# Performance work log

Measured on AMD Instinct MI355X. Metric: run time of the kernel, lower is better.

Reference implementation:

```python
import jax, jax.numpy as jnp
import numpy as np

N_QUBITS = 4 + 4  # 8
N_LAYERS = 4
DIM = 2 ** N_QUBITS


def _apply_1q(state, U, wire):
    # state: (B, 2,...,2) complex; U: (2,2) complex; contract qubit `wire`
    s = jnp.moveaxis(state, wire + 1, -1)
    s = s @ U.T  # out[..., i] = sum_j U[i, j] * s[..., j]
    return jnp.moveaxis(s, -1, wire + 1)


def _apply_cnot(state, c, t):
    s = jnp.moveaxis(state, (c + 1, t + 1), (-2, -1))  # (..., 2c, 2t)
    s = jnp.concatenate([s[..., 0:1, :], s[..., 1:2, ::-1]], axis=-2)
    return jnp.moveaxis(s, (-2, -1), (c + 1, t + 1))


def _quantum_layer(q_in, qw):
    """Batched statevector sim: RY(pi*x) encoding + StronglyEntanglingLayers + <Z_i>."""
    B = q_in.shape[0]
    # RY(a)|0> = cos(a/2)|0> + sin(a/2)|1>, a = pi * x  -> product state
    half = q_in * (jnp.pi / 2)
    qvecs = jnp.stack([jnp.cos(half), jnp.sin(half)], axis=-1).astype(jnp.complex64)  # (B, n, 2)
    state = qvecs[:, 0]
    for i in range(1, N_QUBITS):
        state = (state[:, :, None] * qvecs[:, i][:, None, :]).reshape(B, -1)
    state = state.reshape((B,) + (2,) * N_QUBITS)
    # Rot(phi, theta, omega) = RZ(omega) RY(theta) RZ(phi)
    phi, theta, omega = qw[..., 0], qw[..., 1], qw[..., 2]
    c, s = jnp.cos(theta / 2), jnp.sin(theta / 2)
    m00 = jnp.exp(-0.5j * (phi + omega)) * c
    m01 = -jnp.exp(0.5j * (phi - omega)) * s
    m10 = jnp.exp(-0.5j * (phi - omega)) * s
    m11 = jnp.exp(0.5j * (phi + omega)) * c
    rot = jnp.stack([jnp.stack([m00, m01], -1), jnp.stack([m10, m11], -1)], -2)  # (L, n, 2, 2)
    rot = rot.astype(jnp.complex64)
    for l in range(N_LAYERS):
        for w in range(N_QUBITS):
            state = _apply_1q(state, rot[l, w], w)
        r = (l % (N_QUBITS - 1)) + 1  # PennyLane default ranges
        for w in range(N_QUBITS):
            state = _apply_cnot(state, w, (w + r) % N_QUBITS)
    amps = state.reshape(B, DIM)
    probs = jnp.real(amps * jnp.conj(amps))  # (B, 2^n) float32
    # <Z_i> = sum_b probs_b * (+1 if bit_i(b)==0 else -1); wire 0 = most significant axis
    idx = np.arange(DIM)
    bits = (idx[None, :] >> (N_QUBITS - 1 - np.arange(N_QUBITS))[:, None]) & 1  # (n, 2^n)
    zvals = jnp.asarray(1.0 - 2.0 * bits, dtype=jnp.float32)
    return probs @ zvals.T  # (B, n)


def _forward(x, w_pre1, b_pre1, w_pre2, b_pre2, w_pre3, b_pre3, qw,
             w_post1, b_post1, w_post2, b_post2, w_post3, b_post3):
    # eval mode: dropout is identity
    h = jax.nn.relu(x @ w_pre1 + b_pre1)
    h = jax.nn.relu(h @ w_pre2 + b_pre2)
    q_in = jnp.tanh(h @ w_pre3 + b_pre3)          # (B, n_qubits)
    z = _quantum_layer(q_in, qw)                   # (B, n_qubits)
    h = jax.nn.relu(z @ w_post1 + b_post1)
    h = jax.nn.relu(h @ w_post2 + b_post2)
    return h @ w_post3 + b_post3                   # (B, num_classes)


def setup_inputs() -> dict:
    key = jax.random.key(0)
    ks = jax.random.split(key, 16)
    B, D_IN, C = 16384, 41, 5
    def lin(k, fan_in, fan_out):
        lim = 1.0 / np.sqrt(fan_in)
        k1, k2 = jax.random.split(k)
        return (jax.random.uniform(k1, (fan_in, fan_out), jnp.float32, -lim, lim),
                jax.random.uniform(k2, (fan_out,), jnp.float32, -lim, lim))
    x = jax.random.normal(ks[0], (B, D_IN), jnp.float32)
    w_pre1, b_pre1 = lin(ks[1], D_IN, 64)
    w_pre2, b_pre2 = lin(ks[2], 64, 32)
    w_pre3, b_pre3 = lin(ks[3], 32, N_QUBITS)
    qw = jax.random.normal(ks[4], (N_LAYERS, N_QUBITS, 3), jnp.float32) * 0.1
    w_post1, b_post1 = lin(ks[5], N_QUBITS, 32)
    w_post2, b_post2 = lin(ks[6], 32, 16)
    w_post3, b_post3 = lin(ks[7], 16, C)
    return dict(x=x, w_pre1=w_pre1, b_pre1=b_pre1, w_pre2=w_pre2, b_pre2=b_pre2,
                w_pre3=w_pre3, b_pre3=b_pre3, qw=qw,
                w_post1=w_post1, b_post1=b_post1, w_post2=w_post2, b_post2=b_post2,
                w_post3=w_post3, b_post3=b_post3)


def reference(x, w_pre1, b_pre1, w_pre2, b_pre2, w_pre3, b_pre3, qw,
              w_post1, b_post1, w_post2, b_post2, w_post3, b_post3):
    return _forward(x, w_pre1, b_pre1, w_pre2, b_pre2, w_pre3, b_pre3, qw,
                    w_post1, b_post1, w_post2, b_post2, w_post3, b_post3)
```

## Files before the change

### kernel.cpp

```cpp
#include <hip/hip_runtime.h>
#include <math.h>

#define PI_HALF 1.57079632679489662f

typedef float v2f __attribute__((ext_vector_type(2)));


__device__ __forceinline__ v2f sp(float x) { v2f r; r.x = x; r.y = x; return r; }
__device__ __forceinline__ v2f pkfma(v2f a, v2f b, v2f c) {
  return __builtin_elementwise_fma(a, b, c);
}

template <int CTRL>
__device__ __forceinline__ float dpp_mov(float v) {
  int r = __builtin_amdgcn_update_dpp(0, __float_as_int(v), CTRL, 0xf, 0xf, true);
  return __int_as_float(r);
}
template <int MASK>
__device__ __forceinline__ float lane_xor(float v) {
  if constexpr (MASK == 1) return dpp_mov<0xB1>(v);
  else if constexpr (MASK == 2) return dpp_mov<0x4E>(v);
  else if constexpr (MASK == 8) return dpp_mov<0x128>(v);
  else return dpp_mov<0x1B>(dpp_mov<0x141>(v));
}
template <int MASK>
__device__ __forceinline__ v2f dpp2(v2f v) {
  v2f r; r.x = lane_xor<MASK>(v.x); r.y = lane_xor<MASK>(v.y); return r;
}

template <int W>
__device__ __forceinline__ void rot_lane(v2f (&RE)[8], v2f (&IM)[8],
                                         const float4 mA, int g) {
  constexpr int LM = 1 << (3 - W);
  const unsigned bit = (g >> (3 - W)) & 1u;
  const int sgn = (int)(bit << 31);
  v2f Av = sp(mA.x);
  v2f Bv = sp(__int_as_float(__float_as_int(mA.y) ^ sgn));
  v2f Cv = sp(__int_as_float(__float_as_int(mA.z) ^ sgn));
  v2f Dv = sp(mA.w);
#pragma unroll
  for (int j = 0; j < 8; ++j) {
    v2f pr = dpp2<LM>(RE[j]);
    v2f pi = dpp2<LM>(IM[j]);
    v2f nr = pkfma(-Dv, pi, pkfma(Cv, pr, pkfma(-Bv, IM[j], Av * RE[j])));
    v2f ni = pkfma( Dv, pr, pkfma(Cv, pi, pkfma( Bv, RE[j], Av * IM[j])));
    RE[j] = nr; IM[j] = ni;
  }
}

template <int JM>
__device__ __forceinline__ void rot_regj(v2f (&RE)[8], v2f (&IM)[8],
                                         const float4 mA) {
  v2f M0r = sp(mA.x), M0i = sp(mA.y), M1r = sp(mA.z), M1i = sp(mA.w);
#pragma unroll
  for (int j = 0; j < 8; ++j) {
    if (!(j & JM)) {
      const int j1 = j | JM;
      v2f r0 = RE[j], i0 = IM[j], r1 = RE[j1], i1 = IM[j1];
      RE[j]  = pkfma(-M1i, i1, pkfma(M1r, r1, pkfma(-M0i, i0, M0r * r0)));
      IM[j]  = pkfma( M1i, r1, pkfma(M1r, i1, pkfma( M0i, r0, M0r * i0)));
      RE[j1] = pkfma( M0i, i1, pkfma(M0r, r1, pkfma(-M1i, i0, (-M1r) * r0)));
      IM[j1] = pkfma(-M0i, r1, pkfma(M0r, i1, pkfma( M1i, r0, (-M1r) * i0)));
    }
  }
}

__device__ __forceinline__ void rot_regh(v2f (&RE)[8], v2f (&IM)[8],
                                         const float4 mA) {
#pragma unroll
  for (int j = 0; j < 8; ++j) {
    float r0 = RE[j].x, i0 = IM[j].x, r1 = RE[j].y, i1 = IM[j].y;
    RE[j].x = fmaf(-mA.w, i1, fmaf(mA.z, r1, fmaf(-mA.y, i0, mA.x * r0)));
    IM[j].x = fmaf( mA.w, r1, fmaf(mA.z, i1, fmaf( mA.y, r0, mA.x * i0)));
    RE[j].y = fmaf( mA.y, i1, fmaf(mA.x, r1, fmaf(-mA.w, i0, -mA.z * r0)));
    IM[j].y = fmaf(-mA.y, r1, fmaf(mA.x, i1, fmaf( mA.w, r0, -mA.z * i0)));
  }
}

template <int GPOS, int LM>
__device__ __forceinline__ void cnot_LL(v2f (&RE)[8], v2f (&IM)[8], int g) {
  const bool cb = (g >> GPOS) & 1;
#pragma unroll
  for (int j = 0; j < 8; ++j) {
    v2f pr = dpp2<LM>(RE[j]);
    v2f pi = dpp2<LM>(IM[j]);
    RE[j] = cb ? pr : RE[j];
    IM[j] = cb ? pi : IM[j];
  }
}
template <int GPOS, int JM>
__device__ __forceinline__ void cnot_LR(v2f (&RE)[8], v2f (&IM)[8], int g) {
  const bool cb = (g >> GPOS) & 1;
#pragma unroll
  for (int j = 0; j < 8; ++j) {
    if (!(j & JM)) {
      const int j1 = j | JM;
      v2f r0 = RE[j], r1 = RE[j1];
      RE[j] = cb ? r1 : r0;  RE[j1] = cb ? r0 : r1;
      v2f i0 = IM[j], i1 = IM[j1];
      IM[j] = cb ? i1 : i0;  IM[j1] = cb ? i0 : i1;
    }
  }
}
template <int GPOS>
__device__ __forceinline__ void cnot_LH(v2f (&RE)[8], v2f (&IM)[8], int g) {
  const bool cb = (g >> GPOS) & 1;
#pragma unroll
  for (int j = 0; j < 8; ++j) {
    v2f r = RE[j]; v2f rs; rs.x = r.y; rs.y = r.x;
    RE[j] = cb ? rs : r;
    v2f i = IM[j]; v2f is2; is2.x = i.y; is2.y = i.x;
    IM[j] = cb ? is2 : i;
  }
}
template <int JC, int LM>
__device__ __forceinline__ void cnot_RL(v2f (&RE)[8], v2f (&IM)[8]) {
#pragma unroll
  for (int j = 0; j < 8; ++j) {
    if (j & JC) {
      RE[j] = dpp2<LM>(RE[j]);
      IM[j] = dpp2<LM>(IM[j]);
    }
  }
}
template <int JC>
__device__ __forceinline__ void cnot_RH(v2f (&RE)[8], v2f (&IM)[8]) {
#pragma unroll
  for (int j = 0; j < 8; ++j) {
    if (j & JC) {
      v2f r = RE[j]; RE[j].x = r.y; RE[j].y = r.x;
      v2f i = IM[j]; IM[j].x = i.y; IM[j].y = i.x;
    }
  }
}
template <int LM>
__device__ __forceinline__ void cnot_HL(v2f (&RE)[8], v2f (&IM)[8]) {
#pragma unroll
  for (int j = 0; j < 8; ++j) {
    RE[j].y = lane_xor<LM>(RE[j].y);
    IM[j].y = lane_xor<LM>(IM[j].y);
  }
}
template <int JC, int JT>
__device__ __forceinline__ void cnot_RR(v2f (&RE)[8], v2f (&IM)[8]) {
#pragma unroll
  for (int j = 0; j < 8; ++j) {
    if ((j & JC) && !(j & JT)) {
      const int j1 = j | JT;
      v2f t = RE[j]; RE[j] = RE[j1]; RE[j1] = t;
      t = IM[j]; IM[j] = IM[j1]; IM[j1] = t;
    }
  }
}

__device__ __forceinline__ void stage_fence() { __threadfence_block(); }

__global__ __launch_bounds__(256) void hqc_kernel(
    const float* __restrict__ x,
    const float* __restrict__ w1, const float* __restrict__ b1,
    const float* __restrict__ w2, const float* __restrict__ b2,
    const float* __restrict__ w3, const float* __restrict__ b3,
    const float* __restrict__ qw,
    const float* __restrict__ wp1, const float* __restrict__ bp1,
    const float* __restrict__ wp2, const float* __restrict__ bp2,
    const float* __restrict__ wp3, const float* __restrict__ bp3,
    float* __restrict__ out, int B) {
  __shared__ __align__(16) float rotm[32][4];
  __shared__ float xbuf[16][44];
  __shared__ __align__(16) float hbuf[16][68];
  __shared__ float h2buf[16][34];
  __shared__ float qbuf[16][20];
  __shared__ float p1buf[16][34];
  __shared__ float p2buf[16][20];

  const int tid = threadIdx.x;
  const int g = tid & 15;
  const int ls = tid >> 4;
  const int s = blockIdx.x * 16 + ls;
  const bool valid = (s < B);

  if (tid < 32) {
    float phi = qw[tid * 3 + 0];
    float th  = qw[tid * 3 + 1];
    float om  = qw[tid * 3 + 2];
    float st_, ct; sincosf(0.5f * th, &st_, &ct);
    float sa, ca;  sincosf(0.5f * (phi + om), &sa, &ca);
    float sb, cb;  sincosf(0.5f * (phi - om), &sb, &cb);
    rotm[tid][0] =  ca * ct;
    rotm[tid][1] = -sa * ct;
    rotm[tid][2] = -cb * st_;
    rotm[tid][3] = -sb * st_;
  }

  if (valid) {
    xbuf[ls][g]      = x[s * 41 + g];
    xbuf[ls][g + 16] = x[s * 41 + g + 16];
    if (g < 9) xbuf[ls][g + 32] = x[s * 41 + g + 32];
  }
  __syncthreads();

  const float4* w1v = (const float4*)w1;
  float4 bv = ((const float4*)b1)[g];
  v2f aA; aA.x = bv.x; aA.y = bv.y;
  v2f aB; aB.x = bv.z; aB.y = bv.w;
#pragma unroll 8
  for (int k = 0; k < 41; ++k) {
    float xk = xbuf[ls][k];
    float4 wv = w1v[k * 16 + g];
    v2f w01; w01.x = wv.x; w01.y = wv.y;
    v2f w23; w23.x = wv.z; w23.y = wv.w;
    v2f xv = sp(xk);
    aA = pkfma(xv, w01, aA);
    aB = pkfma(xv, w23, aB);
  }
  float4 st4;
  st4.x = fmaxf(aA.x, 0.f); st4.y = fmaxf(aA.y, 0.f);
  st4.z = fmaxf(aB.x, 0.f); st4.w = fmaxf(aB.y, 0.f);
  *(float4*)(&hbuf[ls][4 * g]) = st4;
  stage_fence();

  const v2f* w2v = (const v2f*)w2;
  v2f a2 = ((const v2f*)b2)[g];
#pragma unroll 8
  for (int k = 0; k < 64; ++k)
    a2 = pkfma(sp(hbuf[ls][k]), w2v[k * 16 + g], a2);
  h2buf[ls][2 * g]     = fmaxf(a2.x, 0.f);
  h2buf[ls][2 * g + 1] = fmaxf(a2.y, 0.f);
  stage_fence();

  if (g < 8) {
    float acc = b3[g];
#pragma unroll
    for (int k = 0; k < 32; ++k) acc = fmaf(h2buf[ls][k], w3[k * 8 + g], acc);
    float q = tanhf(acc);
    float sh, ch; sincosf(q * PI_HALF, &sh, &ch);
    qbuf[ls][g]     = ch;
    qbuf[ls][8 + g] = sh;
  }
  stage_fence();

  float cwv[8], swv[8];
#pragma unroll
  for (int w = 0; w < 8; ++w) { cwv[w] = qbuf[ls][w]; swv[w] = qbuf[ls][8 + w]; }
  float lp = 1.0f;
#pragma unroll
  for (int w = 0; w < 4; ++w) lp *= ((g >> (3 - w)) & 1) ? swv[w] : cwv[w];
  float f45[4];
#pragma unroll
  for (int a = 0; a < 4; ++a)
    f45[a] = ((a & 2) ? swv[4] : cwv[4]) * ((a & 1) ? swv[5] : cwv[5]);
  v2f F67[2];
  F67[0].x = cwv[6] * cwv[7]; F67[0].y = cwv[6] * swv[7];
  F67[1].x = swv[6] * cwv[7]; F67[1].y = swv[6] * swv[7];
  v2f RE[8], IM[8];
#pragma unroll
  for (int j = 0; j < 8; ++j) {
    RE[j] = sp(lp * f45[j >> 1]) * F67[j & 1];
    IM[j] = sp(0.0f);
  }

#define RM(L, W) (*(const float4*)(&rotm[(L) * 8 + (W)][0]))
#define ROTS(L)                                 \
  rot_lane<0>(RE, IM, RM(L, 0), g);             \
  rot_lane<1>(RE, IM, RM(L, 1), g);             \
  rot_lane<2>(RE, IM, RM(L, 2), g);             \
  rot_lane<3>(RE, IM, RM(L, 3), g);             \
  rot_regj<4>(RE, IM, RM(L, 4));                \
  rot_regj<2>(RE, IM, RM(L, 5));                \
  rot_regj<1>(RE, IM, RM(L, 6));                \
  rot_regh(RE, IM, RM(L, 7));

  ROTS(0)
  cnot_LL<3, 4>(RE, IM, g);  cnot_LL<2, 2>(RE, IM, g);
  cnot_LL<1, 1>(RE, IM, g);  cnot_LR<0, 4>(RE, IM, g);
  cnot_RR<4, 2>(RE, IM);     cnot_RR<2, 1>(RE, IM);
  cnot_RH<1>(RE, IM);        cnot_HL<8>(RE, IM);
  ROTS(1)
  cnot_LL<3, 2>(RE, IM, g);  cnot_LL<2, 1>(RE, IM, g);
  cnot_LR<1, 4>(RE, IM, g);  cnot_LR<0, 2>(RE, IM, g);
  cnot_RR<4, 1>(RE, IM);     cnot_RH<2>(RE, IM);
  cnot_RL<1, 8>(RE, IM);     cnot_HL<4>(RE, IM);
  ROTS(2)
  cnot_LL<3, 1>(RE, IM, g);  cnot_LR<2, 4>(RE, IM, g);
  cnot_LR<1, 2>(RE, IM, g);  cnot_LR<0, 1>(RE, IM, g);
  cnot_RH<4>(RE, IM);        cnot_RL<2, 8>(RE, IM);
  cnot_RL<1, 4>(RE, IM);     cnot_HL<2>(RE, IM);
  ROTS(3)
  cnot_LR<3, 4>(RE, IM, g);  cnot_LR<2, 2>(RE, IM, g);
  cnot_LR<1, 1>(RE, IM, g);  cnot_LH<0>(RE, IM, g);
  cnot_RL<4, 8>(RE, IM);     cnot_RL<2, 4>(RE, IM);
  cnot_RL<1, 2>(RE, IM);     cnot_HL<1>(RE, IM);

  v2f pv[8];
#pragma unroll
  for (int j = 0; j < 8; ++j) pv[j] = pkfma(RE[j], RE[j], IM[j] * IM[j]);
  v2f t01 = pv[0] + pv[1], t23 = pv[2] + pv[3];
  v2f t45 = pv[4] + pv[5], t67 = pv[6] + pv[7];
  v2f tlo = t01 + t23, thi = t45 + t67;
  v2f tv = tlo + thi;
  float tot = tv.x + tv.y;
  float s4 = thi.x + thi.y;
  v2f v5 = t23 + t67; float s5 = v5.x + v5.y;
  v2f v6 = (pv[1] + pv[3]) + (pv[5] + pv[7]);
  float s6 = v6.x + v6.y;
  float s7 = tv.y;
  float zp[8];
  zp[0] = ((g >> 3) & 1) ? -tot : tot;
  zp[1] = ((g >> 2) & 1) ? -tot : tot;
  zp[2] = ((g >> 1) & 1) ? -tot : tot;
  zp[3] = (g & 1) ? -tot : tot;
  zp[4] = fmaf(-2.f, s4, tot);
  zp[5] = fmaf(-2.f, s5, tot);
  zp[6] = fmaf(-2.f, s6, tot);
  zp[7] = fmaf(-2.f, s7, tot);
#pragma unroll
  for (int w = 0; w < 8; ++w) zp[w] += lane_xor<1>(zp[w]);
#pragma unroll
  for (int w = 0; w < 8; ++w) zp[w] += lane_xor<2>(zp[w]);
#pragma unroll
  for (int w = 0; w < 8; ++w) zp[w] += lane_xor<4>(zp[w]);
#pragma unroll
  for (int w = 0; w < 8; ++w) zp[w] += lane_xor<8>(zp[w]);

  const v2f* wp1v = (const v2f*)wp1;
  v2f q1 = ((const v2f*)bp1)[g];
#pragma unroll
  for (int k = 0; k < 8; ++k)
    q1 = pkfma(sp(zp[k]), wp1v[k * 16 + g], q1);
  p1buf[ls][2 * g]     = fmaxf(q1.x, 0.f);
  p1buf[ls][2 * g + 1] = fmaxf(q1.y, 0.f);
  stage_fence();

  float q2 = bp2[g];
#pragma unroll
  for (int k = 0; k < 32; ++k) q2 = fmaf(p1buf[ls][k], wp2[k * 16 + g], q2);
  p2buf[ls][g] = fmaxf(q2, 0.f);
  stage_fence();

  if (g < 5 && valid) {
    float o = bp3[g];
#pragma unroll
    for (int k = 0; k < 16; ++k) o = fmaf(p2buf[ls][k], wp3[k * 5 + g], o);
    out[s * 5 + g] = o;
  }
}

extern "C" void kernel_launch(void* const* d_in, const int* in_sizes, int n_in,
                              void* d_out, int out_size, void* d_ws,
                              size_t ws_size, hipStream_t stream) {
  const float* x   = (const float*)d_in[0];
  const float* w1  = (const float*)d_in[1];
  const float* b1  = (const float*)d_in[2];
  const float* w2  = (const float*)d_in[3];
  const float* b2  = (const float*)d_in[4];
  const float* w3  = (const float*)d_in[5];
  const float* b3  = (const float*)d_in[6];
  const float* qw  = (const float*)d_in[7];
  const float* wp1 = (const float*)d_in[8];
  const float* bp1 = (const float*)d_in[9];
  const float* wp2 = (const float*)d_in[10];
  const float* bp2 = (const float*)d_in[11];
  const float* wp3 = (const float*)d_in[12];
  const float* bp3 = (const float*)d_in[13];
  float* out = (float*)d_out;
  const int B = in_sizes[0] / 41;
  const int blocks = (B + 15) / 16;
  hipLaunchKernelGGL(hqc_kernel, dim3(blocks), dim3(256), 0, stream,
                     x, w1, b1, w2, b2, w3, b3, qw,
                     wp1, bp1, wp2, bp2, wp3, bp3, out, B);
}
```

Measured before the change: 42.58 us.

## Spread each sample's statevector over 32 lanes instead of 16

Each sample now uses 32 lanes, each holding 8 amplitudes instead of 16. Qubit 4 moves from registers into the lane dimension. Cross-half exchanges for mask 16 use permlane16_swap where available and ds_swizzle otherwise, and the MLP stages are remapped to 32 lanes per sample. The aim is to halve per-thread register work and raise parallelism, at the cost of twice as many blocks and a slower cross-row lane exchange.

```diff
diff --git a/kernel.cpp b/kernel.cpp
--- a/kernel.cpp
+++ b/kernel.cpp
@@ -4,6 +4,7 @@
 #define PI_HALF 1.57079632679489662f
 
 typedef float v2f __attribute__((ext_vector_type(2)));
+typedef unsigned uv2 __attribute__((ext_vector_type(2)));
 
 
 __device__ __forceinline__ v2f sp(float x) { v2f r; r.x = x; r.y = x; return r; }
@@ -16,32 +17,44 @@
   int r = __builtin_amdgcn_update_dpp(0, __float_as_int(v), CTRL, 0xf, 0xf, true);
   return __int_as_float(r);
 }
+
 template <int MASK>
-__device__ __forceinline__ float lane_xor(float v) {
+__device__ __forceinline__ float lane_xor(float v, bool odd) {
   if constexpr (MASK == 1) return dpp_mov<0xB1>(v);
   else if constexpr (MASK == 2) return dpp_mov<0x4E>(v);
+  else if constexpr (MASK == 4) return dpp_mov<0x1B>(dpp_mov<0x141>(v));
   else if constexpr (MASK == 8) return dpp_mov<0x128>(v);
-  else return dpp_mov<0x1B>(dpp_mov<0x141>(v));
+  else {
+#if __has_builtin(__builtin_amdgcn_permlane16_swap)
+    uv2 r = __builtin_amdgcn_permlane16_swap(__float_as_uint(v),
+                                             __float_as_uint(v), false, false);
+    return __uint_as_float(odd ? r.x : r.y);
+#else
+    return __int_as_float(__builtin_amdgcn_ds_swizzle(__float_as_int(v), 0x401F));
+#endif
+  }
 }
 template <int MASK>
-__device__ __forceinline__ v2f dpp2(v2f v) {
-  v2f r; r.x = lane_xor<MASK>(v.x); r.y = lane_xor<MASK>(v.y); return r;
+__device__ __forceinline__ v2f dpp2(v2f v, bool odd) {
+  v2f r; r.x = lane_xor<MASK>(v.x, odd); r.y = lane_xor<MASK>(v.y, odd);
+  return r;
 }
 
 template <int W>
-__device__ __forceinline__ void rot_lane(v2f (&RE)[8], v2f (&IM)[8],
+__device__ __forceinline__ void rot_lane(v2f (&RE)[4], v2f (&IM)[4],
                                          const float4 mA, int g) {
-  constexpr int LM = 1 << (3 - W);
-  const unsigned bit = (g >> (3 - W)) & 1u;
+  constexpr int LM = 1 << (4 - W);
+  const bool odd = (g >> 4) & 1;
+  const unsigned bit = (g >> (4 - W)) & 1u;
   const int sgn = (int)(bit << 31);
   v2f Av = sp(mA.x);
   v2f Bv = sp(__int_as_float(__float_as_int(mA.y) ^ sgn));
   v2f Cv = sp(__int_as_float(__float_as_int(mA.z) ^ sgn));
   v2f Dv = sp(mA.w);
 #pragma unroll
-  for (int j = 0; j < 8; ++j) {
-    v2f pr = dpp2<LM>(RE[j]);
-    v2f pi = dpp2<LM>(IM[j]);
+  for (int j = 0; j < 4; ++j) {
+    v2f pr = dpp2<LM>(RE[j], odd);
+    v2f pi = dpp2<LM>(IM[j], odd);
     v2f nr = pkfma(-Dv, pi, pkfma(Cv, pr, pkfma(-Bv, IM[j], Av * RE[j])));
     v2f ni = pkfma( Dv, pr, pkfma(Cv, pi, pkfma( Bv, RE[j], Av * IM[j])));
     RE[j] = nr; IM[j] = ni;
@@ -49,11 +62,11 @@
 }
 
 template <int JM>
-__device__ __forceinline__ void rot_regj(v2f (&RE)[8], v2f (&IM)[8],
+__device__ __forceinline__ void rot_regj(v2f (&RE)[4], v2f (&IM)[4],
                                          const float4 mA) {
   v2f M0r = sp(mA.x), M0i = sp(mA.y), M1r = sp(mA.z), M1i = sp(mA.w);
 #pragma unroll
-  for (int j = 0; j < 8; ++j) {
+  for (int j = 0; j < 4; ++j) {
     if (!(j & JM)) {
       const int j1 = j | JM;
       v2f r0 = RE[j], i0 = IM[j], r1 = RE[j1], i1 = IM[j1];
@@ -65,10 +78,10 @@
   }
 }
 
-__device__ __forceinline__ void rot_regh(v2f (&RE)[8], v2f (&IM)[8],
+__device__ __forceinline__ void rot_regh(v2f (&RE)[4], v2f (&IM)[4],
                                          const float4 mA) {
 #pragma unroll
-  for (int j = 0; j < 8; ++j) {
+  for (int j = 0; j < 4; ++j) {
     float r0 = RE[j].x, i0 = IM[j].x, r1 = RE[j].y, i1 = IM[j].y;
     RE[j].x = fmaf(-mA.w, i1, fmaf(mA.z, r1, fmaf(-mA.y, i0, mA.x * r0)));
     IM[j].x = fmaf( mA.w, r1, fmaf(mA.z, i1, fmaf( mA.y, r0, mA.x * i0)));
@@ -78,21 +91,22 @@
 }
 
 template <int GPOS, int LM>
-__device__ __forceinline__ void cnot_LL(v2f (&RE)[8], v2f (&IM)[8], int g) {
+__device__ __forceinline__ void cnot_LL(v2f (&RE)[4], v2f (&IM)[4], int g) {
   const bool cb = (g >> GPOS) & 1;
-#pragma unroll
-  for (int j = 0; j < 8; ++j) {
-    v2f pr = dpp2<LM>(RE[j]);
-    v2f pi = dpp2<LM>(IM[j]);
+  const bool odd = (g >> 4) & 1;
+#pragma unroll
+  for (int j = 0; j < 4; ++j) {
+    v2f pr = dpp2<LM>(RE[j], odd);
+    v2f pi = dpp2<LM>(IM[j], odd);
     RE[j] = cb ? pr : RE[j];
     IM[j] = cb ? pi : IM[j];
   }
 }
 template <int GPOS, int JM>
-__device__ __forceinline__ void cnot_LR(v2f (&RE)[8], v2f (&IM)[8], int g) {
+__device__ __forceinline__ void cnot_LR(v2f (&RE)[4], v2f (&IM)[4], int g) {
   const bool cb = (g >> GPOS) & 1;
 #pragma unroll
-  for (int j = 0; j < 8; ++j) {
+  for (int j = 0; j < 4; ++j) {
     if (!(j & JM)) {
       const int j1 = j | JM;
       v2f r0 = RE[j], r1 = RE[j1];
@@ -103,10 +117,10 @@
   }
 }
 template <int GPOS>
-__device__ __forceinline__ void cnot_LH(v2f (&RE)[8], v2f (&IM)[8], int g) {
+__device__ __forceinline__ void cnot_LH(v2f (&RE)[4], v2f (&IM)[4], int g) {
   const bool cb = (g >> GPOS) & 1;
 #pragma unroll
-  for (int j = 0; j < 8; ++j) {
+  for (int j = 0; j < 4; ++j) {
     v2f r = RE[j]; v2f rs; rs.x = r.y; rs.y = r.x;
     RE[j] = cb ? rs : r;
     v2f i = IM[j]; v2f is2; is2.x = i.y; is2.y = i.x;
@@ -114,19 +128,20 @@
   }
 }
 template <int JC, int LM>
-__device__ __forceinline__ void cnot_RL(v2f (&RE)[8], v2f (&IM)[8]) {
-#pragma unroll
-  for (int j = 0; j < 8; ++j) {
+__device__ __forceinline__ void cnot_RL(v2f (&RE)[4], v2f (&IM)[4], int g) {
+  const bool odd = (g >> 4) & 1;
+#pragma unroll
+  for (int j = 0; j < 4; ++j) {
     if (j & JC) {
-      RE[j] = dpp2<LM>(RE[j]);
-      IM[j] = dpp2<LM>(IM[j]);
+      RE[j] = dpp2<LM>(RE[j], odd);
+      IM[j] = dpp2<LM>(IM[j], odd);
     }
   }
 }
 template <int JC>
-__device__ __forceinline__ void cnot_RH(v2f (&RE)[8], v2f (&IM)[8]) {
-#pragma unroll
-  for (int j = 0; j < 8; ++j) {
+__device__ __forceinline__ void cnot_RH(v2f (&RE)[4], v2f (&IM)[4]) {
+#pragma unroll
+  for (int j = 0; j < 4; ++j) {
     if (j & JC) {
       v2f r = RE[j]; RE[j].x = r.y; RE[j].y = r.x;
       v2f i = IM[j]; IM[j].x = i.y; IM[j].y = i.x;
@@ -134,17 +149,18 @@
   }
 }
 template <int LM>
-__device__ __forceinline__ void cnot_HL(v2f (&RE)[8], v2f (&IM)[8]) {
-#pragma unroll
-  for (int j = 0; j < 8; ++j) {
-    RE[j].y = lane_xor<LM>(RE[j].y);
-    IM[j].y = lane_xor<LM>(IM[j].y);
+__device__ __forceinline__ void cnot_HL(v2f (&RE)[4], v2f (&IM)[4], int g) {
+  const bool odd = (g >> 4) & 1;
+#pragma unroll
+  for (int j = 0; j < 4; ++j) {
+    RE[j].y = lane_xor<LM>(RE[j].y, odd);
+    IM[j].y = lane_xor<LM>(IM[j].y, odd);
   }
 }
 template <int JC, int JT>
-__device__ __forceinline__ void cnot_RR(v2f (&RE)[8], v2f (&IM)[8]) {
-#pragma unroll
-  for (int j = 0; j < 8; ++j) {
+__device__ __forceinline__ void cnot_RR(v2f (&RE)[4], v2f (&IM)[4]) {
+#pragma unroll
+  for (int j = 0; j < 4; ++j) {
     if ((j & JC) && !(j & JT)) {
       const int j1 = j | JT;
       v2f t = RE[j]; RE[j] = RE[j1]; RE[j1] = t;
@@ -166,17 +182,17 @@
     const float* __restrict__ wp3, const float* __restrict__ bp3,
     float* __restrict__ out, int B) {
   __shared__ __align__(16) float rotm[32][4];
-  __shared__ float xbuf[16][44];
-  __shared__ __align__(16) float hbuf[16][68];
-  __shared__ float h2buf[16][34];
-  __shared__ float qbuf[16][20];
-  __shared__ float p1buf[16][34];
-  __shared__ float p2buf[16][20];
+  __shared__ float xbuf[8][44];
+  __shared__ __align__(16) float hbuf[8][68];
+  __shared__ float h2buf[8][34];
+  __shared__ float qbuf[8][20];
+  __shared__ float p1buf[8][34];
+  __shared__ float p2buf[8][20];
 
   const int tid = threadIdx.x;
-  const int g = tid & 15;
-  const int ls = tid >> 4;
-  const int s = blockIdx.x * 16 + ls;
+  const int g = tid & 31;
+  const int ls = tid >> 5;
+  const int s = blockIdx.x * 8 + ls;
   const bool valid = (s < B);
 
   if (tid < 32) {
@@ -193,39 +209,24 @@
   }
 
   if (valid) {
-    xbuf[ls][g]      = x[s * 41 + g];
-    xbuf[ls][g + 16] = x[s * 41 + g + 16];
+    xbuf[ls][g] = x[s * 41 + g];
     if (g < 9) xbuf[ls][g + 32] = x[s * 41 + g + 32];
   }
   __syncthreads();
 
-  const float4* w1v = (const float4*)w1;
-  float4 bv = ((const float4*)b1)[g];
-  v2f aA; aA.x = bv.x; aA.y = bv.y;
-  v2f aB; aB.x = bv.z; aB.y = bv.w;
+  const v2f* w1v = (const v2f*)w1;
+  v2f a1 = ((const v2f*)b1)[g];
 #pragma unroll 8
-  for (int k = 0; k < 41; ++k) {
-    float xk = xbuf[ls][k];
-    float4 wv = w1v[k * 16 + g];
-    v2f w01; w01.x = wv.x; w01.y = wv.y;
-    v2f w23; w23.x = wv.z; w23.y = wv.w;
-    v2f xv = sp(xk);
-    aA = pkfma(xv, w01, aA);
-    aB = pkfma(xv, w23, aB);
-  }
-  float4 st4;
-  st4.x = fmaxf(aA.x, 0.f); st4.y = fmaxf(aA.y, 0.f);
-  st4.z = fmaxf(aB.x, 0.f); st4.w = fmaxf(aB.y, 0.f);
-  *(float4*)(&hbuf[ls][4 * g]) = st4;
-  stage_fence();
-
-  const v2f* w2v = (const v2f*)w2;
-  v2f a2 = ((const v2f*)b2)[g];
+  for (int k = 0; k < 41; ++k)
+    a1 = pkfma(sp(xbuf[ls][k]), w1v[k * 32 + g], a1);
+  v2f st2; st2.x = fmaxf(a1.x, 0.f); st2.y = fmaxf(a1.y, 0.f);
+  *(v2f*)(&hbuf[ls][2 * g]) = st2;
+  stage_fence();
+
+  float a2 = b2[g];
 #pragma unroll 8
-  for (int k = 0; k < 64; ++k)
-    a2 = pkfma(sp(hbuf[ls][k]), w2v[k * 16 + g], a2);
-  h2buf[ls][2 * g]     = fmaxf(a2.x, 0.f);
-  h2buf[ls][2 * g + 1] = fmaxf(a2.y, 0.f);
+  for (int k = 0; k < 64; ++k) a2 = fmaf(hbuf[ls][k], w2[k * 32 + g], a2);
+  h2buf[ls][g] = fmaxf(a2, 0.f);
   stage_fence();
 
   if (g < 8) {
@@ -244,97 +245,94 @@
   for (int w = 0; w < 8; ++w) { cwv[w] = qbuf[ls][w]; swv[w] = qbuf[ls][8 + w]; }
   float lp = 1.0f;
 #pragma unroll
-  for (int w = 0; w < 4; ++w) lp *= ((g >> (3 - w)) & 1) ? swv[w] : cwv[w];
-  float f45[4];
+  for (int w = 0; w < 5; ++w) lp *= ((g >> (4 - w)) & 1) ? swv[w] : cwv[w];
+  float f56[4];
 #pragma unroll
   for (int a = 0; a < 4; ++a)
-    f45[a] = ((a & 2) ? swv[4] : cwv[4]) * ((a & 1) ? swv[5] : cwv[5]);
-  v2f F67[2];
-  F67[0].x = cwv[6] * cwv[7]; F67[0].y = cwv[6] * swv[7];
-  F67[1].x = swv[6] * cwv[7]; F67[1].y = swv[6] * swv[7];
-  v2f RE[8], IM[8];
-#pragma unroll
-  for (int j = 0; j < 8; ++j) {
-    RE[j] = sp(lp * f45[j >> 1]) * F67[j & 1];
+    f56[a] = ((a & 2) ? swv[5] : cwv[5]) * ((a & 1) ? swv[6] : cwv[6]);
+  v2f F7; F7.x = cwv[7]; F7.y = swv[7];
+  v2f RE[4], IM[4];
+#pragma unroll
+  for (int j = 0; j < 4; ++j) {
+    RE[j] = sp(lp * f56[j]) * F7;
     IM[j] = sp(0.0f);
   }
 
 #define RM(L, W) (*(const float4*)(&rotm[(L) * 8 + (W)][0]))
-#define ROTS(L)                                 \
-  rot_lane<0>(RE, IM, RM(L, 0), g);             \
-  rot_lane<1>(RE, IM, RM(L, 1), g);             \
-  rot_lane<2>(RE, IM, RM(L, 2), g);             \
-  rot_lane<3>(RE, IM, RM(L, 3), g);             \
-  rot_regj<4>(RE, IM, RM(L, 4));                \
-  rot_regj<2>(RE, IM, RM(L, 5));                \
-  rot_regj<1>(RE, IM, RM(L, 6));                \
+#define ROTS(L)                          \
+  rot_lane<0>(RE, IM, RM(L, 0), g);      \
+  rot_lane<1>(RE, IM, RM(L, 1), g);      \
+  rot_lane<2>(RE, IM, RM(L, 2), g);      \
+  rot_lane<3>(RE, IM, RM(L, 3), g);      \
+  rot_lane<4>(RE, IM, RM(L, 4), g);      \
+  rot_regj<2>(RE, IM, RM(L, 5));         \
+  rot_regj<1>(RE, IM, RM(L, 6));         \
   rot_regh(RE, IM, RM(L, 7));
 
   ROTS(0)
-  cnot_LL<3, 4>(RE, IM, g);  cnot_LL<2, 2>(RE, IM, g);
-  cnot_LL<1, 1>(RE, IM, g);  cnot_LR<0, 4>(RE, IM, g);
-  cnot_RR<4, 2>(RE, IM);     cnot_RR<2, 1>(RE, IM);
-  cnot_RH<1>(RE, IM);        cnot_HL<8>(RE, IM);
+  cnot_LL<4, 8>(RE, IM, g);  cnot_LL<3, 4>(RE, IM, g);
+  cnot_LL<2, 2>(RE, IM, g);  cnot_LL<1, 1>(RE, IM, g);
+  cnot_LR<0, 2>(RE, IM, g);  cnot_RR<2, 1>(RE, IM);
+  cnot_RH<1>(RE, IM);        cnot_HL<16>(RE, IM, g);
   ROTS(1)
-  cnot_LL<3, 2>(RE, IM, g);  cnot_LL<2, 1>(RE, IM, g);
-  cnot_LR<1, 4>(RE, IM, g);  cnot_LR<0, 2>(RE, IM, g);
-  cnot_RR<4, 1>(RE, IM);     cnot_RH<2>(RE, IM);
-  cnot_RL<1, 8>(RE, IM);     cnot_HL<4>(RE, IM);
+  cnot_LL<4, 4>(RE, IM, g);  cnot_LL<3, 2>(RE, IM, g);
+  cnot_LL<2, 1>(RE, IM, g);  cnot_LR<1, 2>(RE, IM, g);
+  cnot_LR<0, 1>(RE, IM, g);  cnot_RH<2>(RE, IM);
+  cnot_RL<1, 16>(RE, IM, g); cnot_HL<8>(RE, IM, g);
   ROTS(2)
-  cnot_LL<3, 1>(RE, IM, g);  cnot_LR<2, 4>(RE, IM, g);
-  cnot_LR<1, 2>(RE, IM, g);  cnot_LR<0, 1>(RE, IM, g);
-  cnot_RH<4>(RE, IM);        cnot_RL<2, 8>(RE, IM);
-  cnot_RL<1, 4>(RE, IM);     cnot_HL<2>(RE, IM);
+  cnot_LL<4, 2>(RE, IM, g);  cnot_LL<3, 1>(RE, IM, g);
+  cnot_LR<2, 2>(RE, IM, g);  cnot_LR<1, 1>(RE, IM, g);
+  cnot_LH<0>(RE, IM, g);     cnot_RL<2, 16>(RE, IM, g);
+  cnot_RL<1, 8>(RE, IM, g);  cnot_HL<4>(RE, IM, g);
   ROTS(3)
-  cnot_LR<3, 4>(RE, IM, g);  cnot_LR<2, 2>(RE, IM, g);
-  cnot_LR<1, 1>(RE, IM, g);  cnot_LH<0>(RE, IM, g);
-  cnot_RL<4, 8>(RE, IM);     cnot_RL<2, 4>(RE, IM);
-  cnot_RL<1, 2>(RE, IM);     cnot_HL<1>(RE, IM);
-
-  v2f pv[8];
-#pragma unroll
-  for (int j = 0; j < 8; ++j) pv[j] = pkfma(RE[j], RE[j], IM[j] * IM[j]);
-  v2f t01 = pv[0] + pv[1], t23 = pv[2] + pv[3];
-  v2f t45 = pv[4] + pv[5], t67 = pv[6] + pv[7];
-  v2f tlo = t01 + t23, thi = t45 + t67;
-  v2f tv = tlo + thi;
+  cnot_LL<4, 1>(RE, IM, g);  cnot_LR<3, 2>(RE, IM, g);
+  cnot_LR<2, 1>(RE, IM, g);  cnot_LH<1>(RE, IM, g);
+  cnot_LL<0, 16>(RE, IM, g); cnot_RL<2, 8>(RE, IM, g);
+  cnot_RL<1, 4>(RE, IM, g);  cnot_HL<2>(RE, IM, g);
+
+  v2f pv[4];
+#pragma unroll
+  for (int j = 0; j < 4; ++j) pv[j] = pkfma(RE[j], RE[j], IM[j] * IM[j]);
+  v2f tv = (pv[0] + pv[1]) + (pv[2] + pv[3]);
   float tot = tv.x + tv.y;
-  float s4 = thi.x + thi.y;
-  v2f v5 = t23 + t67; float s5 = v5.x + v5.y;
-  v2f v6 = (pv[1] + pv[3]) + (pv[5] + pv[7]);
-  float s6 = v6.x + v6.y;
+  v2f v5 = pv[2] + pv[3]; float s5 = v5.x + v5.y;
+  v2f v6 = pv[1] + pv[3]; float s6 = v6.x + v6.y;
   float s7 = tv.y;
   float zp[8];
-  zp[0] = ((g >> 3) & 1) ? -tot : tot;
-  zp[1] = ((g >> 2) & 1) ? -tot : tot;
-  zp[2] = ((g >> 1) & 1) ? -tot : tot;
-  zp[3] = (g & 1) ? -tot : tot;
-  zp[4] = fmaf(-2.f, s4, tot);
+  zp[0] = ((g >> 4) & 1) ? -tot : tot;
+  zp[1] = ((g >> 3) & 1) ? -tot : tot;
+  zp[2] = ((g >> 2) & 1) ? -tot : tot;
+  zp[3] = ((g >> 1) & 1) ? -tot : tot;
+  zp[4] = (g & 1) ? -tot : tot;
   zp[5] = fmaf(-2.f, s5, tot);
   zp[6] = fmaf(-2.f, s6, tot);
   zp[7] = fmaf(-2.f, s7, tot);
-#pragma unroll
-  for (int w = 0; w < 8; ++w) zp[w] += lane_xor<1>(zp[w]);
-#pragma unroll
-  for (int w = 0; w < 8; ++w) zp[w] += lane_xor<2>(zp[w]);
-#pragma unroll
-  for (int w = 0; w < 8; ++w) zp[w] += lane_xor<4>(zp[w]);
-#pragma unroll
-  for (int w = 0; w < 8; ++w) zp[w] += lane_xor<8>(zp[w]);
-
-  const v2f* wp1v = (const v2f*)wp1;
-  v2f q1 = ((const v2f*)bp1)[g];
-#pragma unroll
-  for (int k = 0; k < 8; ++k)
-    q1 = pkfma(sp(zp[k]), wp1v[k * 16 + g], q1);
-  p1buf[ls][2 * g]     = fmaxf(q1.x, 0.f);
-  p1buf[ls][2 * g + 1] = fmaxf(q1.y, 0.f);
-  stage_fence();
-
-  float q2 = bp2[g];
-#pragma unroll
-  for (int k = 0; k < 32; ++k) q2 = fmaf(p1buf[ls][k], wp2[k * 16 + g], q2);
-  p2buf[ls][g] = fmaxf(q2, 0.f);
+  {
+    const bool odd = (g >> 4) & 1;
+#pragma unroll
+    for (int w = 0; w < 8; ++w) zp[w] += lane_xor<1>(zp[w], odd);
+#pragma unroll
+    for (int w = 0; w < 8; ++w) zp[w] += lane_xor<2>(zp[w], odd);
+#pragma unroll
+    for (int w = 0; w < 8; ++w) zp[w] += lane_xor<4>(zp[w], odd);
+#pragma unroll
+    for (int w = 0; w < 8; ++w) zp[w] += lane_xor<8>(zp[w], odd);
+#pragma unroll
+    for (int w = 0; w < 8; ++w) zp[w] += lane_xor<16>(zp[w], odd);
+  }
+
+  float q1 = bp1[g];
+#pragma unroll
+  for (int k = 0; k < 8; ++k) q1 = fmaf(zp[k], wp1[k * 32 + g], q1);
+  p1buf[ls][g] = fmaxf(q1, 0.f);
+  stage_fence();
+
+  if (g < 16) {
+    float q2 = bp2[g];
+#pragma unroll
+    for (int k = 0; k < 32; ++k) q2 = fmaf(p1buf[ls][k], wp2[k * 16 + g], q2);
+    p2buf[ls][g] = fmaxf(q2, 0.f);
+  }
   stage_fence();
 
   if (g < 5 && valid) {
@@ -364,7 +362,7 @@
   const float* bp3 = (const float*)d_in[13];
   float* out = (float*)d_out;
   const int B = in_sizes[0] / 41;
-  const int blocks = (B + 15) / 16;
+  const int blocks = (B + 7) / 8;
   hipLaunchKernelGGL(hqc_kernel, dim3(blocks), dim3(256), 0, stream,
                      x, w1, b1, w2, b2, w3, b3, qw,
                      wp1, bp1, wp2, bp2, wp3, bp3, out, B);
```

After: 51.72 us. 21.5% more time.
